# Kernel tuning notes

Hardware: AMD Instinct MI355X
Metric: run time of the kernel (lower is better)

## Reference

```python
import jax, jax.numpy as jnp
import numpy as np

DIM = 512
H = 8
HEAD = DIM // H
SCALE = HEAD ** -0.5
B, XL, KL = 4, 1024, 256


def _split(t):
    b, n, _ = t.shape
    return t.reshape(b, n, H, HEAD).transpose(0, 2, 1, 3)


def _merge(t):
    b, h, n, d = t.shape
    return t.transpose(0, 2, 1, 3).reshape(b, n, h * d)


def _qkv(t, W):
    q, k, v = jnp.split(t @ W, 3, axis=-1)
    return _split(q), _split(k), _split(v)


def setup_inputs() -> dict:
    key = jax.random.key(0)
    ks = jax.random.split(key, 20)
    def n(i, shape):
        return jax.random.normal(ks[i], shape, dtype=jnp.float32)
    return {
        "x": n(0, (B, XL, DIM)),
        "kernal": n(1, (B, KL, DIM)),
        "i_x": n(2, (B, XL, DIM)),
        "i_kernal": n(3, (B, KL, DIM)),
        "rd": jax.random.randint(ks[4], (B, KL, XL), 0, 66),
        "polar_pos": jax.random.randint(ks[5], (B, KL, XL), 0, 8),
        "att_mask": jax.random.bernoulli(ks[6], 0.1, (B, H, XL, KL)),
        "i_att_mask": jax.random.bernoulli(ks[7], 0.1, (B, H, XL, KL)),
        "cross_att_mask": jax.random.bernoulli(ks[8], 0.1, (B, H, XL, KL)),
        "Wqkv": n(9, (DIM, 3 * DIM)) * 0.02,
        "Wqkv_i": n(10, (DIM, 3 * DIM)) * 0.02,
        "Wqkv_i2": n(11, (DIM, 3 * DIM)) * 0.02,
        "Wproj": n(12, (DIM, DIM)) * 0.02,
        "bproj": jnp.zeros((DIM,), jnp.float32),
        "Wproj_i": n(13, (DIM, DIM)) * 0.02,
        "bproj_i": jnp.zeros((DIM,), jnp.float32),
        "Wproj_i2": n(14, (DIM, DIM)) * 0.02,
        "bproj_i2": jnp.zeros((DIM,), jnp.float32),
        "dis_embed": n(15, (66, H)) * 0.02,
        "polar_emb": n(16, (8, 1)) * 0.02,
    }


def reference(x, kernal, i_x, i_kernal, rd, polar_pos, att_mask, i_att_mask, cross_att_mask, Wqkv, Wqkv_i, Wqkv_i2, Wproj, bproj, Wproj_i, bproj_i, Wproj_i2, bproj_i2, dis_embed, polar_emb):
    q, k, v = _qkv(x, Wqkv)
    k_q, k_k, k_v = _qkv(kernal, Wqkv)
    i_q, i_k, i_v = _qkv(i_x, Wqkv_i)
    i_k_q, i_k_k, i_k_v = _qkv(i_kernal, Wqkv_i)

    rd_bias = dis_embed[rd].transpose(0, 3, 1, 2)              # [b,h,kl,xl]
    k_x_attn = jnp.einsum('bhkd,bhxd->bhkx', k_q, k) * SCALE   # [b,h,kl,xl]

    # main-orientation: per (b,h,k) sum of |attn| over x grouped by polar bin
    polar = jnp.clip(polar_pos, 0, 7)[:, None, :, :]           # [b,1,kl,xl]
    abs_attn = jnp.abs(k_x_attn)
    ori_sum = jnp.stack([jnp.sum(abs_attn * (polar == o), axis=-1) for o in range(8)], axis=-1)  # [b,h,kl,8]
    main_ori = jnp.argmax(ori_sum, axis=-1)                    # [b,h,kl]
    new_polar = polar - main_ori[..., None]
    new_polar = jnp.where(new_polar < 0, new_polar + 8, new_polar)
    polar_bias = polar_emb[new_polar, 0]                       # [b,h,kl,xl]

    kx = jnp.where(jnp.transpose(att_mask, (0, 1, 3, 2)), -1e6, k_x_attn)
    kx = jax.nn.softmax(kx + rd_bias + polar_bias, axis=-1)
    k_out = _merge(jnp.einsum('bhkx,bhxd->bhkd', kx, v)) @ Wproj + bproj

    x_k = jnp.einsum('bhxd,bhkd->bhxk', q, k_k) * SCALE
    x_k = jnp.where(att_mask, -1e9, x_k)
    x_k = jax.nn.softmax(x_k + jnp.transpose(rd_bias + polar_bias, (0, 1, 3, 2)), axis=-1)
    x_out1 = _merge(jnp.einsum('bhxk,bhkd->bhxd', x_k, k_v)) @ Wproj + bproj

    x_ik = jnp.einsum('bhxd,bhkd->bhxk', q, i_k_k) * SCALE
    x_ik = jax.nn.softmax(jnp.where(cross_att_mask, -1e9, x_ik), axis=-1)
    x_out2 = _merge(jnp.einsum('bhxk,bhkd->bhxd', x_ik, i_k_v)) @ Wproj + bproj
    x_out = x_out1 + x_out2

    ik_ix = jnp.einsum('bhkd,bhxd->bhkx', i_k_q, i_k) * SCALE
    ik_ix = jnp.where(jnp.transpose(i_att_mask, (0, 1, 3, 2)), -1e9, ik_ix)
    ik_ix = jax.nn.softmax(ik_ix, axis=-1)
    i_k_out = _merge(jnp.einsum('bhkx,bhxd->bhkd', ik_ix, i_v)) @ Wproj_i + bproj_i

    i_k2_q, i_k2_k, i_k2_v = _qkv(i_k_out, Wqkv_i2)
    ix_ik2 = jnp.einsum('bhxd,bhkd->bhxk', i_q, i_k2_k) * SCALE
    ix_ik2 = jax.nn.softmax(jnp.where(i_att_mask, -1e9, ix_ik2), axis=-1)
    i_x_out = _merge(jnp.einsum('bhxk,bhkd->bhxd', ix_ik2, i_k2_v)) @ Wproj_i2 + bproj_i2

    return (x_out, k_out, i_x_out)
```

## Files before the change

### kernel.cpp

```cpp
#include <hip/hip_runtime.h>
#include <cstddef>
#include <cstdint>

#define BB 4
#define HH 8
#define HEADD 64
#define DIMM 512
#define XLL 1024
#define KLL 256
#define BHH (BB*HH)

typedef __attribute__((ext_vector_type(8))) short bf16x8;
typedef __attribute__((ext_vector_type(8))) unsigned short u16x8;
typedef __attribute__((ext_vector_type(4))) float f32x4;
typedef unsigned short u16;
typedef unsigned long long u64;

__device__ __forceinline__ u16 f2b(float f) {
    unsigned int u = __builtin_bit_cast(unsigned int, f);
    u = u + 0x7fffu + ((u >> 16) & 1u);
    return (u16)(u >> 16);
}
__device__ __forceinline__ float b2f(u16 h) {
    unsigned int u = ((unsigned int)h) << 16;
    return __builtin_bit_cast(float, u);
}
__device__ __forceinline__ f32x4 mfma16(bf16x8 a, bf16x8 b, f32x4 c) {
    return __builtin_amdgcn_mfma_f32_16x16x32_bf16(a, b, c, 0, 0, 0);
}
__device__ __forceinline__ float wred_max(float v) {
    #pragma unroll
    for (int o = 1; o < 64; o <<= 1) v = fmaxf(v, __shfl_xor(v, o, 64));
    return v;
}
__device__ __forceinline__ float wred_sum(float v) {
    #pragma unroll
    for (int o = 1; o < 64; o <<= 1) v += __shfl_xor(v, o, 64);
    return v;
}


__global__ __launch_bounds__(256) void prep_all_k(
    const float* __restrict__ s0, const float* __restrict__ s1,
    const float* __restrict__ s2, const float* __restrict__ s3,
    const float* __restrict__ s4, const float* __restrict__ s5,
    u16* __restrict__ d0, u16* __restrict__ d1, u16* __restrict__ d2,
    u16* __restrict__ d3, u16* __restrict__ d4, u16* __restrict__ d5,
    const int* __restrict__ i_att, unsigned char* __restrict__ iattT8,
    u16* __restrict__ iattBF,
    const int* __restrict__ cross, u16* __restrict__ crossBF)
{
    const int id = blockIdx.x;
    if (id < 3072) {
        __shared__ float t[32][33];
        const float* W; u16* Wt; int N, bx, by;
        if (id < 2304) {
            int which = id / 768, local = id - which * 768;
            W = which == 0 ? s0 : (which == 1 ? s1 : s2);
            Wt = which == 0 ? d0 : (which == 1 ? d1 : d2);
            N = 1536; bx = local % 48; by = local / 48;
        } else {
            int which = (id - 2304) / 256, local = (id - 2304) % 256;
            W = which == 0 ? s3 : (which == 1 ? s4 : s5);
            Wt = which == 0 ? d3 : (which == 1 ? d4 : d5);
            N = 512; bx = local % 16; by = local / 16;
        }
        const int K = 512;
        int tx = threadIdx.x & 31, ty = threadIdx.x >> 5;
        #pragma unroll
        for (int r = ty; r < 32; r += 8)
            t[r][tx] = W[(size_t)(by * 32 + r) * N + bx * 32 + tx];
        __syncthreads();
        #pragma unroll
        for (int r = ty; r < 32; r += 8)
            Wt[(size_t)(bx * 32 + r) * K + by * 32 + tx] = f2b(t[tx][r]);
        return;
    }
    const int id2 = id - 3072;
    const int xt = id2 & 31, kt = (id2 >> 5) & 7, z = id2 >> 8;
    const int bh = z & 31;
    const int tid = threadIdx.x;
    const u16 NEG = f2b(-1e9f);
    const int sl = tid >> 7, rem = tid & 127, l = rem >> 1, nilow = rem & 1;
    const int lg = l >> 4, lr_ = l & 15;
    const int xl0 = sl * 16 + lg * 4, kl = nilow * 16 + lr_;
    if (z < 32) {
        __shared__ unsigned char t8[32][33];
        const int tx = tid & 31, ty = tid >> 5;
        #pragma unroll
        for (int r = ty; r < 32; r += 8)
            t8[r][tx] = (unsigned char)(i_att[((size_t)bh * 1024 + xt * 32 + r) * 256 + kt * 32 + tx] != 0);
        __syncthreads();
        #pragma unroll
        for (int r = ty; r < 32; r += 8)
            iattT8[((size_t)bh * 256 + kt * 32 + r) * 1024 + xt * 32 + tx] = t8[tx][r];
        ushort4 o;
        o.x = t8[xl0 + 0][kl] ? NEG : (u16)0;
        o.y = t8[xl0 + 1][kl] ? NEG : (u16)0;
        o.z = t8[xl0 + 2][kl] ? NEG : (u16)0;
        o.w = t8[xl0 + 3][kl] ? NEG : (u16)0;
        size_t eb = (((size_t)bh * 64 + xt * 2 + sl) * 8 + kt) * 512 + (size_t)l * 8 + nilow * 4;
        *reinterpret_cast<ushort4*>(iattBF + eb) = o;
    } else {
        const int kg = kt * 32 + kl;
        u16 o_[4];
        #pragma unroll
        for (int j = 0; j < 4; ++j) {
            int mm = cross[((size_t)bh * 1024 + xt * 32 + xl0 + j) * 256 + kg];
            o_[j] = mm ? NEG : (u16)0;
        }
        ushort4 o; o.x = o_[0]; o.y = o_[1]; o.z = o_[2]; o.w = o_[3];
        size_t eb = (((size_t)bh * 64 + xt * 2 + sl) * 8 + kt) * 512 + (size_t)l * 8 + nilow * 4;
        *reinterpret_cast<ushort4*>(crossBF + eb) = o;
    }
}

__global__ __launch_bounds__(256) void main_ori_k8(
    const u16* __restrict__ S, const int* __restrict__ polar,
    int* __restrict__ MO)
{
    const int blk = blockIdx.x;
    const int b = blk >> 8, k = blk & 255;
    const int tid = threadIdx.x;
    const int wave = tid >> 6, lane = tid & 63;
    const int c = tid * 4;
    int4 p4 = *reinterpret_cast<const int4*>(polar + ((size_t)b * 256 + k) * 1024 + c);
    int pp[4] = { p4.x, p4.y, p4.z, p4.w };
    #pragma unroll
    for (int j = 0; j < 4; ++j) { int p = pp[j]; pp[j] = p < 0 ? 0 : (p > 7 ? 7 : p); }
    __shared__ float sred[4][8];
    for (int h = 0; h < 8; ++h) {
        const int bh = b * 8 + h;
        ushort4 sv = *reinterpret_cast<const ushort4*>(S + ((size_t)bh * 256 + k) * 1024 + c);
        float av[4] = { fabsf(b2f(sv.x)), fabsf(b2f(sv.y)), fabsf(b2f(sv.z)), fabsf(b2f(sv.w)) };
        float bins[8] = {};
        #pragma unroll
        for (int j = 0; j < 4; ++j) {
            #pragma unroll
            for (int o = 0; o < 8; ++o) bins[o] += (pp[j] == o) ? av[j] : 0.0f;
        }
        #pragma unroll
        for (int o = 0; o < 8; ++o) bins[o] = wred_sum(bins[o]);
        if (lane == 0) {
            #pragma unroll
            for (int o = 0; o < 8; ++o) sred[wave][o] = bins[o];
        }
        __syncthreads();
        if (tid == 0) {
            int best = 0; float bv = -1.0f;
            #pragma unroll
            for (int o = 0; o < 8; ++o) {
                float s = sred[0][o] + sred[1][o] + sred[2][o] + sred[3][o];
                if (s > bv) { bv = s; best = o; }
            }
            MO[bh * 256 + k] = best;
        }
        __syncthreads();
    }
}

__global__ __launch_bounds__(256) void bias_build_k(
    const int* __restrict__ rd, const int* __restrict__ polar,
    const int* __restrict__ att, const float* __restrict__ dis,
    const float* __restrict__ pemb, const int* __restrict__ MO,
    u16* __restrict__ biasF, u16* __restrict__ bias1)
{
    const int b = blockIdx.z;
    const int xt = blockIdx.x * 32, kt = blockIdx.y * 32;
    const int tid = threadIdx.x;
    __shared__ float dsh[528];
    __shared__ int rds[32][33];
    __shared__ int pls[32][33];
    __shared__ u16 bt[32][33];
    for (int i = tid; i < 528; i += 256) dsh[i] = dis[i];
    const int tx = tid & 31, ty = tid >> 5;
    #pragma unroll
    for (int r = ty; r < 32; r += 8) {
        size_t src = ((size_t)b * 256 + kt + r) * 1024 + xt + tx;
        rds[tx][r] = rd[src];
        int p = polar[src]; pls[tx][r] = p < 0 ? 0 : (p > 7 ? 7 : p);
    }
    float pe[8];
    #pragma unroll
    for (int o = 0; o < 8; ++o) pe[o] = pemb[o];
    __syncthreads();
    const int sl = tid >> 7, rem = tid & 127, l = rem >> 1, nilow = rem & 1;
    const int lg = l >> 4, lr_ = l & 15;
    const int xl0 = sl * 16 + lg * 4, kl = nilow * 16 + lr_;
    const int kg = kt + kl;
    const u16 NEG9 = f2b(-1e9f), NEG6 = f2b(-1e6f);
    for (int h = 0; h < 8; ++h) {
        const int bh = b * 8 + h;
        int mo = MO[bh * 256 + kg];
        u16 o9[4];
        #pragma unroll
        for (int j = 0; j < 4; ++j) {
            int xl = xl0 + j;
            int mm = att[((size_t)bh * 1024 + xt + xl) * 256 + kg];
            float v = dsh[rds[xl][kl] * 8 + h] + pe[(pls[xl][kl] - mo + 8) & 7];
            u16 vb = f2b(v);
            o9[j] = mm ? NEG9 : vb;
            bt[xl][kl] = mm ? NEG6 : vb;
        }
        size_t eb = (((size_t)bh * 64 + (xt >> 4) + sl) * 8 + (kt >> 5)) * 512 + (size_t)l * 8 + nilow * 4;
        ushort4 ov; ov.x = o9[0]; ov.y = o9[1]; ov.z = o9[2]; ov.w = o9[3];
        *reinterpret_cast<ushort4*>(biasF + eb) = ov;
        __syncthreads();
        const int k_ = tid >> 3, x4 = (tid & 7) * 4;
        ushort4 o2;
        o2.x = bt[x4 + 0][k_]; o2.y = bt[x4 + 1][k_];
        o2.z = bt[x4 + 2][k_]; o2.w = bt[x4 + 3][k_];
        *reinterpret_cast<ushort4*>(bias1 + ((size_t)bh * 256 + kt + k_) * 1024 + xt + x4) = o2;
        __syncthreads();
    }
}

template<typename AT>
__device__ __forceinline__ void gemm_core_128(
    const AT* __restrict__ A, const AT* __restrict__ A2,
    const u16* __restrict__ Wt,
    int rb, int cb, short* Asl, short* Bsl, f32x4 (&acc)[4][4])
{
    constexpr bool F32 = sizeof(AT) == 4;
    const int tid = threadIdx.x;
    const int w = tid >> 6, lane = tid & 63;
    const int lr = lane & 15, lk = (lane >> 4) * 8;
    const int wr = (w >> 1) * 64, wc = (w & 1) * 64;
    const int srow = tid >> 3, skc = (tid & 7) * 8;
    const AT* gA = A + (size_t)(rb + srow) * 512 + skc;
    const AT* gA2 = A2 ? A2 + (size_t)(rb + srow) * 512 + skc : nullptr;
    const u16* gB = Wt + (size_t)(cb + srow) * 512 + skc;
    float4 ral[4], rah[4];
    bf16x8 rab[4], rab2[4], rw[4];
    #pragma unroll
    for (int it = 0; it < 4; ++it) {
        if constexpr (F32) {
            ral[it] = *reinterpret_cast<const float4*>(gA + (size_t)it * 32 * 512);
            rah[it] = *reinterpret_cast<const float4*>(gA + (size_t)it * 32 * 512 + 4);
        } else {
            rab[it] = *reinterpret_cast<const bf16x8*>(gA + (size_t)it * 32 * 512);
            if (gA2) rab2[it] = *reinterpret_cast<const bf16x8*>(gA2 + (size_t)it * 32 * 512);
        }
        rw[it] = *reinterpret_cast<const bf16x8*>(gB + (size_t)it * 32 * 512);
    }
    for (int t = 0; t < 8; ++t) {
        #pragma unroll
        for (int it = 0; it < 4; ++it) {
            if constexpr (F32) {
                u16x8 o;
                o[0] = f2b(ral[it].x); o[1] = f2b(ral[it].y);
                o[2] = f2b(ral[it].z); o[3] = f2b(ral[it].w);
                o[4] = f2b(rah[it].x); o[5] = f2b(rah[it].y);
                o[6] = f2b(rah[it].z); o[7] = f2b(rah[it].w);
                *reinterpret_cast<u16x8*>(&Asl[(it * 32 + srow) * 72 + skc]) = o;
            } else {
                if (gA2) {
                    u16x8 o;
                    #pragma unroll
                    for (int e = 0; e < 8; ++e)
                        o[e] = f2b(b2f((u16)rab[it][e]) + b2f((u16)rab2[it][e]));
                    *reinterpret_cast<u16x8*>(&Asl[(it * 32 + srow) * 72 + skc]) = o;
                } else {
                    *reinterpret_cast<bf16x8*>(&Asl[(it * 32 + srow) * 72 + skc]) = rab[it];
                }
            }
            *reinterpret_cast<bf16x8*>(&Bsl[(it * 32 + srow) * 72 + skc]) = rw[it];
        }
        if (t < 7) {
            const int k0 = (t + 1) * 64;
            #pragma unroll
            for (int it = 0; it < 4; ++it) {
                if constexpr (F32) {
                    ral[it] = *reinterpret_cast<const float4*>(gA + k0 + (size_t)it * 32 * 512);
                    rah[it] = *reinterpret_cast<const float4*>(gA + k0 + (size_t)it * 32 * 512 + 4);
                } else {
                    rab[it] = *reinterpret_cast<const bf16x8*>(gA + k0 + (size_t)it * 32 * 512);
                    if (gA2) rab2[it] = *reinterpret_cast<const bf16x8*>(gA2 + k0 + (size_t)it * 32 * 512);
                }
                rw[it] = *reinterpret_cast<const bf16x8*>(gB + k0 + (size_t)it * 32 * 512);
            }
        }
        __syncthreads();
        #pragma unroll
        for (int ks = 0; ks < 2; ++ks) {
            bf16x8 af[4], bf_[4];
            #pragma unroll
            for (int mi = 0; mi < 4; ++mi)
                af[mi] = *reinterpret_cast<const bf16x8*>(&Asl[(wr + mi * 16 + lr) * 72 + ks * 32 + lk]);
            #pragma unroll
            for (int ni = 0; ni < 4; ++ni)
                bf_[ni] = *reinterpret_cast<const bf16x8*>(&Bsl[(wc + ni * 16 + lr) * 72 + ks * 32 + lk]);
            #pragma unroll
            for (int mi = 0; mi < 4; ++mi)
                #pragma unroll
                for (int ni = 0; ni < 4; ++ni)
                    acc[mi][ni] = mfma16(af[mi], bf_[ni], acc[mi][ni]);
        }
        __syncthreads();
    }
}

template<typename AT>
__device__ __forceinline__ void qkv_body(
    const AT* __restrict__ A, const u16* __restrict__ Wt,
    u16* __restrict__ qb, u16* __restrict__ kb, u16* __restrict__ vt,
    int sl, int rb, int cb)
{
    __shared__ __align__(16) short Ls[2 * 128 * 72];
    short* Asl = Ls;
    short* Bsl = Ls + 128 * 72;
    f32x4 acc[4][4] = {};
    gemm_core_128<AT>(A, nullptr, Wt, rb, cb, Asl, Bsl, acc);
    const int tid = threadIdx.x;
    const int wave = tid >> 6, lane = tid & 63;
    const int lr = lane & 15, lg = lane >> 4;
    const int wr = (wave >> 1) * 64, wc = (wave & 1) * 64;
    const int seq = 1 << sl, smask = seq - 1;
    if (cb < 1024) {
        const float scl = (cb < 512) ? 0.125f : 1.0f;
        #pragma unroll
        for (int mi = 0; mi < 4; ++mi)
            #pragma unroll
            for (int ni = 0; ni < 4; ++ni) {
                int row = wr + mi * 16 + lg * 4;
                int col = wc + ni * 16 + lr;
                f32x4 v = acc[mi][ni];
                #pragma unroll
                for (int j = 0; j < 4; ++j)
                    Ls[(row + j) * 136 + col] = (short)f2b(v[j] * scl);
            }
        __syncthreads();
        u16* dst = (cb < 512) ? qb : kb;
        if (dst) {
            const int cbase = (cb < 512) ? cb : cb - 512;
            #pragma unroll
            for (int p = 0; p < 8; ++p) {
                int slot = p * 256 + tid;
                int row = slot >> 4;
                int half = (slot >> 3) & 1;
                int inner = slot & 7;
                int m = rb + row;
                int bb = m >> sl, n = m & smask;
                int cg = cbase + half * 64;
                int h = cg >> 6;
                u16x8 val = *reinterpret_cast<u16x8*>(&Ls[row * 136 + half * 64 + inner * 8]);
                *reinterpret_cast<u16x8*>(
                    &dst[(((size_t)bb * HH + h) * seq + n) * 64 + inner * 8]) = val;
            }
        }
    } else {
        #pragma unroll
        for (int mi = 0; mi < 4; ++mi)
            #pragma unroll
            for (int ni = 0; ni < 4; ++ni) {
                int col = wc + ni * 16 + lr;
                int row0 = wr + mi * 16 + lg * 4;
                f32x4 v = acc[mi][ni];
                #pragma unroll
                for (int j = 0; j < 4; ++j)
                    Ls[col * 136 + row0 + j] = (short)f2b(v[j]);
            }
        __syncthreads();
        const int bb = rb >> sl, n0 = rb & smask;
        #pragma unroll
        for (int p = 0; p < 4; ++p) {
            int slot = p * 256 + tid;
            int col = slot >> 3;
            int inner = slot & 7;
            int dg = (cb - 1024) + col;
            int h = dg >> 6, d = dg & 63;
            u16* vrow = vt + ((((size_t)bb * HH + h) * 64 + d) << sl) + n0;
            u16x8 v0 = *reinterpret_cast<u16x8*>(&Ls[col * 136 + inner * 8]);
            u16x8 v1 = *reinterpret_cast<u16x8*>(&Ls[col * 136 + 64 + inner * 8]);
            *reinterpret_cast<u16x8*>(vrow + inner * 8) = v0;
            *reinterpret_cast<u16x8*>(vrow + 64 + inner * 8) = v1;
        }
    }
}

__global__ __launch_bounds__(256, 3) void gemm_qkv_all_k(
    const float* __restrict__ A0, const float* __restrict__ A1,
    const float* __restrict__ A2, const float* __restrict__ A3,
    const u16* __restrict__ W01, const u16* __restrict__ W23,
    u16* q0, u16* k0, u16* v0, u16* q1, u16* k1, u16* v1,
    u16* q2, u16* k2, u16* v2, u16* q3, u16* k3, u16* v3)
{
    const int lin = blockIdx.x;
    const int swz = (lin & 7) * 120 + (lin >> 3);
    const int x = swz % 12, y = swz / 12;
    const float* A; const u16* Wt; u16 *qb, *kb, *vt; int sl, ry;
    if (y < 32)      { A = A0; Wt = W01; qb = q0; kb = k0; vt = v0; sl = 10; ry = y; }
    else if (y < 40) { A = A1; Wt = W01; qb = q1; kb = k1; vt = v1; sl = 8;  ry = y - 32; }
    else if (y < 72) { A = A2; Wt = W23; qb = q2; kb = k2; vt = v2; sl = 10; ry = y - 40; }
    else             { A = A3; Wt = W23; qb = q3; kb = k3; vt = v3; sl = 8;  ry = y - 72; }
    qkv_body<float>(A, Wt, qb, kb, vt, sl, ry * 128, x * 128);
}

__global__ __launch_bounds__(256, 3) void gemm_qkv2_k(
    const u16* __restrict__ A, const u16* __restrict__ Wt,
    u16* kb, u16* vt)
{
    qkv_body<u16>(A, Wt, nullptr, kb, vt, 8, blockIdx.y * 128, (blockIdx.x + 4) * 128);
}

template<bool OUTBF>
__device__ __forceinline__ void proj_body(
    const u16* __restrict__ A, const u16* __restrict__ A2,
    const u16* __restrict__ Wt,
    const float* __restrict__ bias, float bscale, void* __restrict__ outp,
    int rb, int cb)
{
    __shared__ __align__(16) short Ls[2 * 128 * 72];
    f32x4 acc[4][4] = {};
    gemm_core_128<u16>(A, A2, Wt, rb, cb, Ls, Ls + 128 * 72, acc);
    const int tid = threadIdx.x;
    const int wave = tid >> 6, lane = tid & 63;
    const int lr = lane & 15;
    const int wr = (wave >> 1) * 64, wc = (wave & 1) * 64;
    #pragma unroll
    for (int mi = 0; mi < 4; ++mi) {
        int m0 = rb + wr + mi * 16 + (lane >> 4) * 4;
        #pragma unroll
        for (int ni = 0; ni < 4; ++ni) {
            int c = cb + wc + ni * 16 + lr;
            float bv = bscale * bias[c];
            f32x4 v = acc[mi][ni];
            #pragma unroll
            for (int j = 0; j < 4; ++j) {
                size_t o = (size_t)(m0 + j) * 512 + c;
                if (OUTBF) reinterpret_cast<u16*>(outp)[o] = f2b(v[j] + bv);
                else       reinterpret_cast<float*>(outp)[o] = v[j] + bv;
            }
        }
    }
}

__global__ __launch_bounds__(256, 3) void gemm_proj_bf16_k(
    const u16* __restrict__ A, const u16* __restrict__ Wt,
    const float* __restrict__ bias, float bscale, u16* __restrict__ outp)
{
    proj_body<true>(A, nullptr, Wt, bias, bscale, outp, blockIdx.y * 128, blockIdx.x * 128);
}

__global__ __launch_bounds__(256, 3) void gemm_proj3_k(
    const u16* __restrict__ A0, const u16* __restrict__ A0b,
    const u16* __restrict__ A1, const u16* __restrict__ A2,
    const u16* __restrict__ W, const u16* __restrict__ Wi2,
    const float* __restrict__ bp, const float* __restrict__ bpi2,
    float* __restrict__ o0, float* __restrict__ o1, float* __restrict__ o2)
{
    const int id = blockIdx.x;
    const u16 *A, *Ax; const u16* Wt; const float* bias; float bscale; float* outp; int x, y;
    if (id < 128)      { A = A0; Ax = A0b; Wt = W;   bias = bp;   bscale = 2.0f; outp = o0; x = id & 3; y = id >> 2; }
    else if (id < 256) { A = A1; Ax = nullptr; Wt = Wi2; bias = bpi2; bscale = 1.0f; outp = o1; x = (id - 128) & 3; y = (id - 128) >> 2; }
    else               { A = A2; Ax = nullptr; Wt = W;   bias = bp;   bscale = 1.0f; outp = o2; x = (id - 256) & 3; y = (id - 256) >> 2; }
    proj_body<false>(A, Ax, Wt, bias, bscale, outp, y * 128, x * 128);
}

__global__ __launch_bounds__(256, 4) void scores_pair_k(
    const u16* __restrict__ A1, const u16* __restrict__ B1, u16* __restrict__ S1,
    const u16* __restrict__ A2, const u16* __restrict__ B2, u16* __restrict__ S2)
{
    __shared__ __align__(16) short Ls[2 * 128 * 72];
    short* As = Ls;
    short* Bs = Ls + 128 * 72;
    const int z = blockIdx.z, bh = z & 31;
    const u16* Aq = (z < 32) ? A1 : A2;
    const u16* Bk = (z < 32) ? B1 : B2;
    u16* S = (z < 32) ? S1 : S2;
    const int tid = threadIdx.x;
    const int wave = tid >> 6, lane = tid & 63;
    const int lr = lane & 15, lg = lane >> 4, lk = lg * 8;
    const int rb = blockIdx.y * 128, cb = blockIdx.x * 128;
    const int wr = (wave >> 1) * 64, wc = (wave & 1) * 64;
    const u16* Ap = Aq + (size_t)bh * 256 * 64;
    const u16* Bp = Bk + (size_t)bh * 1024 * 64;
    const int srow = tid >> 3, skc = (tid & 7) * 8;
    #pragma unroll
    for (int it = 0; it < 4; ++it) {
        int row = it * 32 + srow;
        *reinterpret_cast<bf16x8*>(&As[row * 72 + skc]) =
            *reinterpret_cast<const bf16x8*>(Ap + (size_t)(rb + row) * 64 + skc);
        *reinterpret_cast<bf16x8*>(&Bs[row * 72 + skc]) =
            *reinterpret_cast<const bf16x8*>(Bp + (size_t)(cb + row) * 64 + skc);
    }
    __syncthreads();
    f32x4 acc[4][4] = {};
    #pragma unroll
    for (int ks = 0; ks < 2; ++ks) {
        bf16x8 af[4], bf_[4];
        #pragma unroll
        for (int mi = 0; mi < 4; ++mi)
            af[mi] = *reinterpret_cast<const bf16x8*>(&As[(wr + mi * 16 + lr) * 72 + ks * 32 + lk]);
        #pragma unroll
        for (int ni = 0; ni < 4; ++ni)
            bf_[ni] = *reinterpret_cast<const bf16x8*>(&Bs[(wc + ni * 16 + lr) * 72 + ks * 32 + lk]);
        #pragma unroll
        for (int mi = 0; mi < 4; ++mi)
            #pragma unroll
            for (int ni = 0; ni < 4; ++ni)
                acc[mi][ni] = mfma16(af[mi], bf_[ni], acc[mi][ni]);
    }
    __syncthreads();
    #pragma unroll
    for (int mi = 0; mi < 4; ++mi)
        #pragma unroll
        for (int ni = 0; ni < 4; ++ni) {
            int row = wr + mi * 16 + lg * 4;
            int col = wc + ni * 16 + lr;
            f32x4 v = acc[mi][ni];
            #pragma unroll
            for (int j = 0; j < 4; ++j)
                Ls[(row + j) * 136 + col] = (short)f2b(v[j]);
        }
    __syncthreads();
    #pragma unroll
    for (int p = 0; p < 8; ++p) {
        int slot = p * 256 + tid;
        int row = slot >> 4;
        int chunk = slot & 15;
        u16x8 val = *reinterpret_cast<u16x8*>(&Ls[row * 136 + chunk * 8]);
        *reinterpret_cast<u16x8*>(
            &S[((size_t)bh * 256 + rb + row) * 1024 + cb + chunk * 8]) = val;
    }
}

template<bool HASB>
__device__ __forceinline__ void pv_fused_body(
    const u16* __restrict__ P, const u16* __restrict__ BIAS,
    const unsigned char* __restrict__ MSK,
    const u16* __restrict__ V, u16* __restrict__ out, short* Ps)
{
    const int tid = threadIdx.x;
    const int wave = tid >> 6, lane = tid & 63;
    const int lr = lane & 15, lg = lane >> 4, lk = lg * 8;
    const int bh = blockIdx.y, b = bh >> 3, h = bh & 7;
    const int rb = blockIdx.x * 64;
    const int wr = wave * 16;
    const size_t rowg = (size_t)bh * 256 + rb + wr + lr;
    const u16* Prow = P + rowg * 1024;
    const u16* Brow = HASB ? BIAS + rowg * 1024 : nullptr;
    const unsigned char* Mrow = HASB ? nullptr : MSK + rowg * 1024;
    const u16* Vb = V + (size_t)bh * 64 * 1024;

    float m = -3.4e38f;
    for (int c0 = 0; c0 < 1024; c0 += 64) {
        #pragma unroll
        for (int ks = 0; ks < 2; ++ks) {
            const int cc = c0 + ks * 32 + lk;
            bf16x8 sv = *reinterpret_cast<const bf16x8*>(Prow + cc);
            if (HASB) {
                bf16x8 bv = *reinterpret_cast<const bf16x8*>(Brow + cc);
                #pragma unroll
                for (int e = 0; e < 8; ++e)
                    m = fmaxf(m, b2f((u16)sv[e]) + b2f((u16)bv[e]));
            } else {
                u64 mk = *reinterpret_cast<const u64*>(Mrow + cc);
                #pragma unroll
                for (int e = 0; e < 8; ++e) {
                    float s = ((mk >> (e * 8)) & 0xFFull) ? -1e9f : b2f((u16)sv[e]);
                    m = fmaxf(m, s);
                }
            }
        }
    }
    m = fmaxf(m, __shfl_xor(m, 16, 64));
    m = fmaxf(m, __shfl_xor(m, 32, 64));

    f32x4 acc[4] = {};
    float sum = 0.0f;
    for (int c0 = 0; c0 < 1024; c0 += 64) {
        #pragma unroll
        for (int ks = 0; ks < 2; ++ks) {
            const int cc = c0 + ks * 32 + lk;
            bf16x8 sv = *reinterpret_cast<const bf16x8*>(Prow + cc);
            bf16x8 ap;
            if (HASB) {
                bf16x8 bv = *reinterpret_cast<const bf16x8*>(Brow + cc);
                #pragma unroll
                for (int e = 0; e < 8; ++e) {
                    float ev = __expf(b2f((u16)sv[e]) + b2f((u16)bv[e]) - m);
                    sum += ev;
                    ap[e] = (short)f2b(ev);
                }
            } else {
                u64 mk = *reinterpret_cast<const u64*>(Mrow + cc);
                #pragma unroll
                for (int e = 0; e < 8; ++e) {
                    float s = ((mk >> (e * 8)) & 0xFFull) ? -1e9f : b2f((u16)sv[e]);
                    float ev = __expf(s - m);
                    sum += ev;
                    ap[e] = (short)f2b(ev);
                }
            }
            #pragma unroll
            for (int ni = 0; ni < 4; ++ni) {
                bf16x8 vv = *reinterpret_cast<const bf16x8*>(
                    Vb + (size_t)(ni * 16 + lr) * 1024 + cc);
                acc[ni] = mfma16(ap, vv, acc[ni]);
            }
        }
    }
    sum += __shfl_xor(sum, 16, 64);
    sum += __shfl_xor(sum, 32, 64);
    const float inv = 1.0f / sum;
    float invj[4];
    #pragma unroll
    for (int j = 0; j < 4; ++j) invj[j] = __shfl(inv, lg * 4 + j, 64);

    short* myP = &Ps[wave * 16 * 72];
    #pragma unroll
    for (int ni = 0; ni < 4; ++ni) {
        int d = ni * 16 + lr;
        f32x4 v = acc[ni];
        #pragma unroll
        for (int j = 0; j < 4; ++j)
            myP[(lg * 4 + j) * 72 + d] = (short)f2b(v[j] * invj[j]);
    }
    #pragma unroll
    for (int p = 0; p < 2; ++p) {
        int slot = p * 64 + lane;
        int rloc = slot >> 3;
        int inner = slot & 7;
        int r0 = rb + wr + rloc;
        u16x8 val = *reinterpret_cast<u16x8*>(&myP[rloc * 72 + inner * 8]);
        *reinterpret_cast<u16x8*>(
            &out[((size_t)(b * 256 + r0)) * 512 + h * 64 + inner * 8]) = val;
    }
}

__global__ __launch_bounds__(256, 4) void pv_fused_k(
    const u16* __restrict__ P1, const u16* __restrict__ B1,
    const u16* __restrict__ V1, u16* __restrict__ o1,
    const u16* __restrict__ P2, const unsigned char* __restrict__ M2,
    const u16* __restrict__ V2, u16* __restrict__ o2)
{
    __shared__ __align__(16) short Ps[4 * 16 * 72];
    if (blockIdx.z == 0)
        pv_fused_body<true>(P1, B1, nullptr, V1, o1, Ps);
    else
        pv_fused_body<false>(P2, nullptr, M2, V2, o2, Ps);
}

__global__ __launch_bounds__(256, 4) void attn_all_k(
    const u16* __restrict__ Q0, const u16* __restrict__ IQ0,
    const u16* __restrict__ K1, const u16* __restrict__ V1t,
    const u16* __restrict__ B1F, u16* __restrict__ out1,
    const u16* __restrict__ K2, const u16* __restrict__ V2t,
    const u16* __restrict__ B2F, u16* __restrict__ out2,
    const u16* __restrict__ K3, const u16* __restrict__ V3t,
    const u16* __restrict__ B3F, u16* __restrict__ out3)
{
    const int tid = threadIdx.x;
    const int w = tid >> 6, lane = tid & 63;
    const int lr = lane & 15, lg = lane >> 4, lk = lg * 8;
    int lin = blockIdx.x;
    const u16 *Qp, *Kp, *Vp, *BF; u16* outm;
    if (lin < 512)        { Qp = Q0;  Kp = K1; Vp = V1t; BF = B1F; outm = out1; }
    else if (lin < 1024)  { Qp = Q0;  Kp = K2; Vp = V2t; BF = B2F; outm = out2; lin -= 512; }
    else                  { Qp = IQ0; Kp = K3; Vp = V3t; BF = B3F; outm = out3; lin -= 1024; }
    const int xcd = lin & 7, idx = lin >> 3;
    const int bh = xcd * 4 + (idx & 3);
    const int rb = (idx >> 2) * 64;
    const int b = bh >> 3, h = bh & 7;
    const int wr = w * 16;
    const int strip = (rb >> 4) + w;

    __shared__ __align__(16) short Ps[4 * 16 * 264];
    short* myP = &Ps[w * 16 * 264];

    bf16x8 qf0, qf1;
    {
        const u16* Qb = Qp + ((size_t)bh * 1024 + rb + wr + lr) * 64;
        qf0 = *reinterpret_cast<const bf16x8*>(Qb + lk);
        qf1 = *reinterpret_cast<const bf16x8*>(Qb + 32 + lk);
    }

    bf16x8 breg[8];
    {
        const u16* bb = BF + (((size_t)bh * 64 + strip) * 8) * 512 + (size_t)lane * 8;
        #pragma unroll
        for (int itp = 0; itp < 8; ++itp)
            breg[itp] = *reinterpret_cast<const bf16x8*>(bb + (size_t)itp * 512);
    }
    const u16* Kb = Kp + (size_t)bh * 256 * 64;
    f32x4 acc[16];
    #pragma unroll
    for (int ni = 0; ni < 16; ++ni) acc[ni] = (f32x4){0.f, 0.f, 0.f, 0.f};
    #pragma unroll
    for (int ni = 0; ni < 16; ++ni) {
        bf16x8 b0 = *reinterpret_cast<const bf16x8*>(Kb + (size_t)(ni * 16 + lr) * 64 + lk);
        acc[ni] = mfma16(qf0, b0, acc[ni]);
    }
    #pragma unroll
    for (int ni = 0; ni < 16; ++ni) {
        bf16x8 b1 = *reinterpret_cast<const bf16x8*>(Kb + (size_t)(ni * 16 + lr) * 64 + 32 + lk);
        acc[ni] = mfma16(qf1, b1, acc[ni]);
    }
    float mx[4] = { -3.4e38f, -3.4e38f, -3.4e38f, -3.4e38f };
    #pragma unroll
    for (int ni = 0; ni < 16; ++ni) {
        const bf16x8 br = breg[ni >> 1];
        #pragma unroll
        for (int j = 0; j < 4; ++j) {
            float v = acc[ni][j] + b2f((u16)br[(ni & 1) * 4 + j]);
            acc[ni][j] = v;
            mx[j] = fmaxf(mx[j], v);
        }
    }
    #pragma unroll
    for (int j = 0; j < 4; ++j) {
        #pragma unroll
        for (int o = 1; o < 16; o <<= 1) mx[j] = fmaxf(mx[j], __shfl_xor(mx[j], o, 64));
    }
    float sm[4] = {};
    #pragma unroll
    for (int ni = 0; ni < 16; ++ni) {
        #pragma unroll
        for (int j = 0; j < 4; ++j) {
            float e = __expf(acc[ni][j] - mx[j]);
            acc[ni][j] = e;
            sm[j] += e;
        }
    }
    #pragma unroll
    for (int j = 0; j < 4; ++j) {
        #pragma unroll
        for (int o = 1; o < 16; o <<= 1) sm[j] += __shfl_xor(sm[j], o, 64);
        sm[j] = 1.0f / sm[j];
    }
    #pragma unroll
    for (int ni = 0; ni < 16; ++ni)
        #pragma unroll
        for (int j = 0; j < 4; ++j)
            myP[(lg * 4 + j) * 264 + ni * 16 + lr] = (short)f2b(acc[ni][j] * sm[j]);
    f32x4 acc2[4] = {};
    #pragma unroll
    for (int kc = 0; kc < 8; ++kc) {
        bf16x8 ap = *reinterpret_cast<const bf16x8*>(&myP[lr * 264 + kc * 32 + lk]);
        #pragma unroll
        for (int ni = 0; ni < 4; ++ni) {
            bf16x8 vv = *reinterpret_cast<const bf16x8*>(
                Vp + ((size_t)bh * 64 + ni * 16 + lr) * 256 + kc * 32 + lk);
            acc2[ni] = mfma16(ap, vv, acc2[ni]);
        }
    }
    #pragma unroll
    for (int ni = 0; ni < 4; ++ni) {
        int d = ni * 16 + lr;
        f32x4 v = acc2[ni];
        #pragma unroll
        for (int j = 0; j < 4; ++j)
            myP[(lg * 4 + j) * 72 + d] = (short)f2b(v[j]);
    }
    #pragma unroll
    for (int p = 0; p < 2; ++p) {
        int slot = p * 64 + lane;
        int rloc = slot >> 3;
        int inner = slot & 7;
        int row = rb + wr + rloc;
        u16x8 val = *reinterpret_cast<u16x8*>(&myP[rloc * 72 + inner * 8]);
        *reinterpret_cast<u16x8*>(
            &outm[((size_t)(b * 1024 + row)) * 512 + h * 64 + inner * 8]) = val;
    }
}

extern "C" void kernel_launch(void* const* d_in, const int* in_sizes, int n_in,
                              void* d_out, int out_size, void* d_ws, size_t ws_size,
                              hipStream_t stream)
{
    const float* x        = (const float*)d_in[0];
    const float* kernal   = (const float*)d_in[1];
    const float* i_x      = (const float*)d_in[2];
    const float* i_kernal = (const float*)d_in[3];
    const int*   rd       = (const int*)d_in[4];
    const int*   polar    = (const int*)d_in[5];
    const int*   att      = (const int*)d_in[6];
    const int*   i_att    = (const int*)d_in[7];
    const int*   cross    = (const int*)d_in[8];
    const float* Wqkv     = (const float*)d_in[9];
    const float* Wqkv_i   = (const float*)d_in[10];
    const float* Wqkv_i2  = (const float*)d_in[11];
    const float* Wproj    = (const float*)d_in[12];
    const float* bproj    = (const float*)d_in[13];
    const float* Wproj_i  = (const float*)d_in[14];
    const float* bproj_i  = (const float*)d_in[15];
    const float* Wproj_i2 = (const float*)d_in[16];
    const float* bproj_i2 = (const float*)d_in[17];
    const float* dis      = (const float*)d_in[18];
    const float* pemb     = (const float*)d_in[19];

    float* out = (float*)d_out;
    float* x_out   = out;
    float* k_out   = out + (size_t)BB * XLL * DIMM;
    float* i_x_out = k_out + (size_t)BB * KLL * DIMM;

    char* ws = (char*)d_ws;
    size_t off = 0;
    auto alloc = [&](size_t bytes) { void* p = ws + off; off += (bytes + 255) & ~(size_t)255; return p; };

    const size_t NAX = (size_t)BB * XLL * DIMM;
    const size_t NAK = (size_t)BB * KLL * DIMM;
    const size_t NHX = (size_t)BHH * XLL * HEADD;
    const size_t NHK = (size_t)BHH * KLL * HEADD;
    const size_t NS  = (size_t)BHH * KLL * XLL;

    u16* WqkvT    = (u16*)alloc((size_t)1536 * 512 * 2);
    u16* WqkvIT   = (u16*)alloc((size_t)1536 * 512 * 2);
    u16* WqkvI2T  = (u16*)alloc((size_t)1536 * 512 * 2);
    u16* WprojT   = (u16*)alloc((size_t)512 * 512 * 2);
    u16* WprojIT  = (u16*)alloc((size_t)512 * 512 * 2);
    u16* WprojI2T = (u16*)alloc((size_t)512 * 512 * 2);
    u16* Q    = (u16*)alloc(NHX * 2);
    u16* KX   = (u16*)alloc(NHX * 2);
    u16* VXt  = (u16*)alloc(NHX * 2);
    u16* IQ   = (u16*)alloc(NHX * 2);
    u16* IK   = (u16*)alloc(NHX * 2);
    u16* IVt  = (u16*)alloc(NHX * 2);
    u16* KQ   = (u16*)alloc(NHK * 2);
    u16* KK   = (u16*)alloc(NHK * 2);
    u16* KVt  = (u16*)alloc(NHK * 2);
    u16* IKQ  = (u16*)alloc(NHK * 2);
    u16* IKK  = (u16*)alloc(NHK * 2);
    u16* IKVt = (u16*)alloc(NHK * 2);
    u16* K2K  = (u16*)alloc(NHK * 2);
    u16* K2Vt = (u16*)alloc(NHK * 2);
    u16* SPa  = (u16*)alloc(NS * 2);
    u16* SPb  = (u16*)alloc(NS * 2);
    u16* KMb  = (u16*)alloc(NAK * 2);
    u16* KMb2 = (u16*)alloc(NAK * 2);
    u16* XMb  = (u16*)alloc(NAX * 2);
    u16* XMb2 = (u16*)alloc(NAX * 2);
    u16* XMc  = (u16*)alloc(NAX * 2);
    u16* IKOUTb = (u16*)alloc(NAK * 2);
    u16* biasF = (u16*)alloc(NS * 2);
    u16* bias1 = (u16*)alloc(NS * 2);
    u16* crossBF = (u16*)alloc(NS * 2);
    u16* iattBF  = (u16*)alloc(NS * 2);
    unsigned char* iattT8 = (unsigned char*)alloc(NS);
    int* MO   = (int*)alloc((size_t)BHH * KLL * 4);

    dim3 blk(256);

    prep_all_k<<<dim3(19456), blk, 0, stream>>>(
        Wqkv, Wqkv_i, Wqkv_i2, Wproj, Wproj_i, Wproj_i2,
        WqkvT, WqkvIT, WqkvI2T, WprojT, WprojIT, WprojI2T,
        i_att, iattT8, iattBF, cross, crossBF);

    gemm_qkv_all_k<<<dim3(960), blk, 0, stream>>>(
        x, kernal, i_x, i_kernal, WqkvT, WqkvIT,
        Q, KX, VXt, KQ, KK, KVt, IQ, IK, IVt, IKQ, IKK, IKVt);

    scores_pair_k<<<dim3(8, 2, 64), blk, 0, stream>>>(KQ, KX, SPa, IKQ, IK, SPb);
    main_ori_k8<<<dim3(BB * KLL), blk, 0, stream>>>(SPa, polar, MO);
    bias_build_k<<<dim3(32, 8, BB), blk, 0, stream>>>(rd, polar, att, dis, pemb, MO, biasF, bias1);
    pv_fused_k<<<dim3(4, 32, 2), blk, 0, stream>>>(
        SPa, bias1, VXt, KMb, SPb, iattT8, IVt, KMb2);
    gemm_proj_bf16_k<<<dim3(4, 8), blk, 0, stream>>>(KMb2, WprojIT, bproj_i, 1.0f, IKOUTb);
    gemm_qkv2_k<<<dim3(8, 8), blk, 0, stream>>>(IKOUTb, WqkvI2T, K2K, K2Vt);
    attn_all_k<<<dim3(1536), blk, 0, stream>>>(
        Q, IQ, KK, KVt, biasF, XMb, IKK, IKVt, crossBF, XMc,
        K2K, K2Vt, iattBF, XMb2);
    gemm_proj3_k<<<dim3(288), blk, 0, stream>>>(
        XMb, XMc, XMb2, KMb, WprojT, WprojI2T, bproj, bproj_i2, x_out, i_x_out, k_out);

    (void)in_sizes; (void)n_in; (void)out_size; (void)ws_size;
}
```

Baseline: 249.9 us.

## Convert cross-attention kernel to chunked online softmax to cut LDS and registers

The attention kernel used to compute all 256 keys' scores at once, keep 16 accumulators and 8 bias registers per lane, and stage the full probability row in LDS. It now processes keys in four chunks of 64 with a running max and sum (online softmax), rescales the output accumulator each chunk and normalizes at the end. This shrinks the per-block LDS buffer and the register footprint, which should allow higher occupancy. In exchange it adds rescale multiplies, extra exps and cross-lane shuffles for every chunk, and serializes the work into four dependent steps.

```diff
diff --git a/kernel.cpp b/kernel.cpp
--- a/kernel.cpp
+++ b/kernel.cpp
@@ -666,8 +666,8 @@
     const int wr = w * 16;
     const int strip = (rb >> 4) + w;
 
-    __shared__ __align__(16) short Ps[4 * 16 * 264];
-    short* myP = &Ps[w * 16 * 264];
+    __shared__ __align__(16) short Ps[4 * 16 * 72];
+    short* myP = &Ps[w * 16 * 72];
 
     bf16x8 qf0, qf1;
     {
@@ -675,83 +675,100 @@
         qf0 = *reinterpret_cast<const bf16x8*>(Qb + lk);
         qf1 = *reinterpret_cast<const bf16x8*>(Qb + 32 + lk);
     }
-
-    bf16x8 breg[8];
-    {
-        const u16* bb = BF + (((size_t)bh * 64 + strip) * 8) * 512 + (size_t)lane * 8;
-        #pragma unroll
-        for (int itp = 0; itp < 8; ++itp)
-            breg[itp] = *reinterpret_cast<const bf16x8*>(bb + (size_t)itp * 512);
-    }
+    const u16* bb = BF + (((size_t)bh * 64 + strip) * 8) * 512 + (size_t)lane * 8;
     const u16* Kb = Kp + (size_t)bh * 256 * 64;
-    f32x4 acc[16];
-    #pragma unroll
-    for (int ni = 0; ni < 16; ++ni) acc[ni] = (f32x4){0.f, 0.f, 0.f, 0.f};
-    #pragma unroll
-    for (int ni = 0; ni < 16; ++ni) {
-        bf16x8 b0 = *reinterpret_cast<const bf16x8*>(Kb + (size_t)(ni * 16 + lr) * 64 + lk);
-        acc[ni] = mfma16(qf0, b0, acc[ni]);
-    }
-    #pragma unroll
-    for (int ni = 0; ni < 16; ++ni) {
-        bf16x8 b1 = *reinterpret_cast<const bf16x8*>(Kb + (size_t)(ni * 16 + lr) * 64 + 32 + lk);
-        acc[ni] = mfma16(qf1, b1, acc[ni]);
-    }
-    float mx[4] = { -3.4e38f, -3.4e38f, -3.4e38f, -3.4e38f };
-    #pragma unroll
-    for (int ni = 0; ni < 16; ++ni) {
-        const bf16x8 br = breg[ni >> 1];
+    const u16* Vb = Vp + (size_t)bh * 64 * 256;
+
+    f32x4 acc2[4] = {};
+    float mrun[4] = { -3.4e38f, -3.4e38f, -3.4e38f, -3.4e38f };
+    float sumr[4] = {};
+    #pragma unroll
+    for (int c = 0; c < 4; ++c) {
+        bf16x8 br0 = *reinterpret_cast<const bf16x8*>(bb + (size_t)(c * 2 + 0) * 512);
+        bf16x8 br1 = *reinterpret_cast<const bf16x8*>(bb + (size_t)(c * 2 + 1) * 512);
+        f32x4 acc[4];
+        #pragma unroll
+        for (int ni = 0; ni < 4; ++ni) acc[ni] = (f32x4){0.f, 0.f, 0.f, 0.f};
+        #pragma unroll
+        for (int ni = 0; ni < 4; ++ni) {
+            bf16x8 b0 = *reinterpret_cast<const bf16x8*>(
+                Kb + (size_t)((c * 4 + ni) * 16 + lr) * 64 + lk);
+            acc[ni] = mfma16(qf0, b0, acc[ni]);
+        }
+        #pragma unroll
+        for (int ni = 0; ni < 4; ++ni) {
+            bf16x8 b1 = *reinterpret_cast<const bf16x8*>(
+                Kb + (size_t)((c * 4 + ni) * 16 + lr) * 64 + 32 + lk);
+            acc[ni] = mfma16(qf1, b1, acc[ni]);
+        }
+        float mx[4] = { -3.4e38f, -3.4e38f, -3.4e38f, -3.4e38f };
+        #pragma unroll
+        for (int ni = 0; ni < 4; ++ni) {
+            const bf16x8 br = (ni < 2) ? br0 : br1;
+            #pragma unroll
+            for (int j = 0; j < 4; ++j) {
+                float v = acc[ni][j] + b2f((u16)br[(ni & 1) * 4 + j]);
+                acc[ni][j] = v;
+                mx[j] = fmaxf(mx[j], v);
+            }
+        }
         #pragma unroll
         for (int j = 0; j < 4; ++j) {
-            float v = acc[ni][j] + b2f((u16)br[(ni & 1) * 4 + j]);
-            acc[ni][j] = v;
-            mx[j] = fmaxf(mx[j], v);
-        }
-    }
-    #pragma unroll
-    for (int j = 0; j < 4; ++j) {
-        #pragma unroll
-        for (int o = 1; o < 16; o <<= 1) mx[j] = fmaxf(mx[j], __shfl_xor(mx[j], o, 64));
-    }
-    float sm[4] = {};
-    #pragma unroll
-    for (int ni = 0; ni < 16; ++ni) {
+            #pragma unroll
+            for (int o = 1; o < 16; o <<= 1) mx[j] = fmaxf(mx[j], __shfl_xor(mx[j], o, 64));
+        }
+        float sc[4];
         #pragma unroll
         for (int j = 0; j < 4; ++j) {
-            float e = __expf(acc[ni][j] - mx[j]);
-            acc[ni][j] = e;
-            sm[j] += e;
-        }
-    }
-    #pragma unroll
-    for (int j = 0; j < 4; ++j) {
-        #pragma unroll
-        for (int o = 1; o < 16; o <<= 1) sm[j] += __shfl_xor(sm[j], o, 64);
-        sm[j] = 1.0f / sm[j];
-    }
-    #pragma unroll
-    for (int ni = 0; ni < 16; ++ni)
-        #pragma unroll
-        for (int j = 0; j < 4; ++j)
-            myP[(lg * 4 + j) * 264 + ni * 16 + lr] = (short)f2b(acc[ni][j] * sm[j]);
-    f32x4 acc2[4] = {};
-    #pragma unroll
-    for (int kc = 0; kc < 8; ++kc) {
-        bf16x8 ap = *reinterpret_cast<const bf16x8*>(&myP[lr * 264 + kc * 32 + lk]);
-        #pragma unroll
-        for (int ni = 0; ni < 4; ++ni) {
-            bf16x8 vv = *reinterpret_cast<const bf16x8*>(
-                Vp + ((size_t)bh * 64 + ni * 16 + lr) * 256 + kc * 32 + lk);
-            acc2[ni] = mfma16(ap, vv, acc2[ni]);
-        }
-    }
+            float m = fmaxf(mrun[j], mx[j]);
+            sc[j] = __expf(mrun[j] - m);
+            mrun[j] = m;
+        }
+        #pragma unroll
+        for (int ni = 0; ni < 4; ++ni)
+            #pragma unroll
+            for (int j = 0; j < 4; ++j) acc2[ni][j] *= sc[j];
+        float sml[4] = {};
+        #pragma unroll
+        for (int ni = 0; ni < 4; ++ni)
+            #pragma unroll
+            for (int j = 0; j < 4; ++j) {
+                float e = __expf(acc[ni][j] - mrun[j]);
+                acc[ni][j] = e;
+                sml[j] += e;
+            }
+        #pragma unroll
+        for (int j = 0; j < 4; ++j) {
+            #pragma unroll
+            for (int o = 1; o < 16; o <<= 1) sml[j] += __shfl_xor(sml[j], o, 64);
+            sumr[j] = sumr[j] * sc[j] + sml[j];
+        }
+        #pragma unroll
+        for (int ni = 0; ni < 4; ++ni)
+            #pragma unroll
+            for (int j = 0; j < 4; ++j)
+                myP[(lg * 4 + j) * 72 + ni * 16 + lr] = (short)f2b(acc[ni][j]);
+        #pragma unroll
+        for (int kc = 0; kc < 2; ++kc) {
+            bf16x8 ap = *reinterpret_cast<const bf16x8*>(&myP[lr * 72 + kc * 32 + lk]);
+            #pragma unroll
+            for (int ni = 0; ni < 4; ++ni) {
+                bf16x8 vv = *reinterpret_cast<const bf16x8*>(
+                    Vb + (size_t)(ni * 16 + lr) * 256 + c * 64 + kc * 32 + lk);
+                acc2[ni] = mfma16(ap, vv, acc2[ni]);
+            }
+        }
+    }
+    float inv[4];
+    #pragma unroll
+    for (int j = 0; j < 4; ++j) inv[j] = 1.0f / sumr[j];
     #pragma unroll
     for (int ni = 0; ni < 4; ++ni) {
         int d = ni * 16 + lr;
         f32x4 v = acc2[ni];
         #pragma unroll
         for (int j = 0; j < 4; ++j)
-            myP[(lg * 4 + j) * 72 + d] = (short)f2b(v[j]);
+            myP[(lg * 4 + j) * 72 + d] = (short)f2b(v[j] * inv[j]);
     }
     #pragma unroll
     for (int p = 0; p < 2; ++p) {
```

Result: no change. 253.1 us (+1.3%).
